# Performance work log

Measured on AMD Instinct MI355X. Metric: run time of the kernel, lower is better.

Reference implementation:

```python
import jax, jax.numpy as jnp
import numpy as np

C = 512
NH = 8
HD = C // NH              # head dim = 64
TOPK = int(HD * 2 / 3)    # keep top-2/3 entries per attention row (DRSformer-style)


def conv2d(x, w, b, groups=1, pad=0):
    y = jax.lax.conv_general_dilated(
        x, w, window_strides=(1, 1), padding=[(pad, pad), (pad, pad)],
        dimension_numbers=('NCHW', 'OIHW', 'NCHW'), feature_group_count=groups)
    return y + b[None, :, None, None]


def setup_inputs() -> dict:
    key = jax.random.key(0)
    ks = jax.random.split(key, 8)
    s = lambda k, sh, fan: jax.random.normal(k, sh, jnp.float32) * (1.0 / np.sqrt(fan))
    return {
        'x': jax.random.normal(ks[0], (2, C, 128, 128), jnp.float32),
        'w_qkv': s(ks[1], (3 * C, C, 1, 1), C),          # 1x1 conv C -> 3C
        'b_qkv': jnp.zeros((3 * C,), jnp.float32),
        'w_dw': s(ks[2], (3 * C, 1, 3, 3), 9),           # 3x3 depthwise on 3C
        'b_dw': jnp.zeros((3 * C,), jnp.float32),
        'scale': jnp.asarray(HD ** -0.5, jnp.float32),   # learned scalar temperature
        'w_proj': s(ks[3], (C, C, 1, 1), C),             # output 1x1 conv
        'b_proj': jnp.zeros((C,), jnp.float32),
    }


def reference(x, w_qkv, b_qkv, w_dw, b_dw, scale, w_proj, b_proj):
    B, _, H, W = x.shape
    # qkv generator: 1x1 conv then 3x3 depthwise conv (Restormer-style)
    qkv = conv2d(x, w_qkv, b_qkv)
    qkv = conv2d(qkv, w_dw, b_dw, groups=3 * C, pad=1)
    q, k, v = jnp.split(qkv, 3, axis=1)
    # b (nh c) h w -> b nh c (h w)
    rs = lambda t: t.reshape(B, NH, HD, H * W)
    q, k, v = rs(q), rs(k), rs(v)
    # L2-normalize along spatial (token) dim
    q = q / jnp.maximum(jnp.linalg.norm(q, axis=-1, keepdims=True), 1e-12)
    k = k / jnp.maximum(jnp.linalg.norm(k, axis=-1, keepdims=True), 1e-12)
    # transposed (channel) attention: [B, NH, HD, HD]
    att = jnp.einsum('bhcn,bhdn->bhcd', q, k) * scale
    # sparsify: keep top-k per row, mask rest to -inf, then softmax
    thresh = jax.lax.top_k(att, TOPK)[0][..., -1:]
    att = jnp.where(att >= thresh, att, -jnp.inf)
    att = jax.nn.softmax(att, axis=-1)
    out = jnp.einsum('bhcd,bhdn->bhcn', att, v)  # [B, NH, HD, HW]
    out = out.reshape(B, C, H, W)
    return conv2d(out, w_proj, b_proj)
```

## Files before the change

kernel.cpp:

```cpp
#include <hip/hip_runtime.h>

typedef unsigned short u16;
typedef _Float16 f16x8 __attribute__((ext_vector_type(8)));
typedef u16 u16x8 __attribute__((ext_vector_type(8)));
typedef u16 u16x4 __attribute__((ext_vector_type(4)));
typedef float f32x4 __attribute__((ext_vector_type(4)));

#define NTOK 16384
#define CCH 512
#define SXN ((long)CCH * NTOK)
#define SQK (512L * NTOK)
#define SQP (1024L * NTOK)
#define SAR 32768L
#define SMB (512L * 512)

__device__ __forceinline__ float h2f(u16 u) {
  _Float16 h = *(_Float16*)&u; return (float)h;
}
__device__ __forceinline__ u16 f2h(float f) {
  _Float16 h = (_Float16)f; return *(u16*)&h;
}
__device__ __forceinline__ void split2(float v, u16& hi, u16& lo) {
  hi = f2h(v); lo = f2h(v - h2f(hi));
}
__device__ __forceinline__ int swz(int row, int ko) { return ko ^ ((row & 7) << 3); }

__device__ __forceinline__ int k2swz(int r, int x) {
  int s = x >> 2, e = x & 3;
  int ps = (((s >> 2) + r) & 7) | ((s & 3) << 3);
  return r * 128 + (ps << 2) + e;
}

__global__ __launch_bounds__(256) void k0_transpose(
    const float* __restrict__ x, u16* __restrict__ xh) {
  __shared__ float ld[64][65];
  const long bz = blockIdx.z;
  x += bz * SXN; xh += bz * SQK;
  const int t = threadIdx.x;
  const int n0 = blockIdx.x * 64, c0 = blockIdx.y * 64;
#pragma unroll
  for (int j = 0; j < 4; ++j) {
    int idx = t + 256 * j;
    int cl = idx >> 4, ns = (idx & 15) * 4;
    float4 v = *(const float4*)(x + (long)(c0 + cl) * NTOK + n0 + ns);
    ld[cl][ns] = v.x; ld[cl][ns + 1] = v.y; ld[cl][ns + 2] = v.z; ld[cl][ns + 3] = v.w;
  }
  __syncthreads();
#pragma unroll
  for (int j = 0; j < 4; ++j) {
    int idx = t + 256 * j;
    int nl = idx >> 4, cs = (idx & 15) * 4;
    u16x4 h;
#pragma unroll
    for (int e = 0; e < 4; ++e) h[e] = f2h(ld[cs + e][nl]);
    *(u16x4*)(xh + (long)(n0 + nl) * CCH + c0 + cs) = h;
  }
}

__global__ __launch_bounds__(256) void k0_cvt_w(const float* __restrict__ a,
                                                u16* __restrict__ oh,
                                                u16* __restrict__ ol) {
  int i = blockIdx.x * 256 + threadIdx.x;
  const float4 v = ((const float4*)a)[i];
  u16 h0, l0, h1, l1, h2, l2, h3, l3;
  split2(v.x, h0, l0); split2(v.y, h1, l1);
  split2(v.z, h2, l2); split2(v.w, h3, l3);
  ((unsigned long long*)oh)[i] = (unsigned long long)h0 | ((unsigned long long)h1 << 16)
                               | ((unsigned long long)h2 << 32) | ((unsigned long long)h3 << 48);
  ((unsigned long long*)ol)[i] = (unsigned long long)l0 | ((unsigned long long)l1 << 16)
                               | ((unsigned long long)l2 << 32) | ((unsigned long long)l3 << 48);
}

__device__ __forceinline__ void storeC(u16* p, float v) { *p = f2h(v); }
__device__ __forceinline__ void storeC(float* p, float v) { *p = v; }

template <typename OutT, bool BIAS_ROW, int GRP, bool GRP_IS_M>
__global__ __launch_bounds__(256) void gemm_bt(
    const u16* __restrict__ A, const u16* __restrict__ B, OutT* __restrict__ C,
    const float* __restrict__ bias, int ldc, long sA, long sB, long sC) {
  const int K = 512;
  __shared__ __align__(16) u16 lA[128 * 64];
  __shared__ __align__(16) u16 lB[128 * 64];
  const long bz = blockIdx.z;
  A += bz * sA; B += bz * sB; C += bz * sC;
  const int t = threadIdx.x;
  const int lane = t & 63, w = t >> 6;
  const int wm = w & 1, wn = w >> 1;
  const int fx = blockIdx.x, fy = blockIdx.y;
  const int gg = fy & (GRP - 1);
  const int go = fx + 8 * (fy / GRP);
  const int bm = (GRP_IS_M ? gg : go) * 128;
  const int bn = (GRP_IS_M ? go : gg) * 128;
  const f32x4 zero4 = {0.f, 0.f, 0.f, 0.f};
  f32x4 acc[4][4];
#pragma unroll
  for (int i = 0; i < 4; ++i)
#pragma unroll
    for (int j = 0; j < 4; ++j) acc[i][j] = zero4;

  for (int kt = 0; kt < K; kt += 64) {
    u16x8 ra[4], rb[4];
#pragma unroll
    for (int j = 0; j < 4; ++j) {
      int idx = t + 256 * j;
      int row = idx >> 3, ko = (idx & 7) << 3;
      ra[j] = *(const u16x8*)(A + (long)(bm + row) * K + kt + ko);
      rb[j] = *(const u16x8*)(B + (long)(bn + row) * K + kt + ko);
    }
    __syncthreads();
#pragma unroll
    for (int j = 0; j < 4; ++j) {
      int idx = t + 256 * j;
      int row = idx >> 3, ko = (idx & 7) << 3;
      *(u16x8*)(&lA[row * 64 + swz(row, ko)]) = ra[j];
      *(u16x8*)(&lB[row * 64 + swz(row, ko)]) = rb[j];
    }
    __syncthreads();
#pragma unroll
    for (int kk = 0; kk < 2; ++kk) {
      f16x8 af[4], bfr[4];
#pragma unroll
      for (int f = 0; f < 4; ++f) {
        int ar = wm * 64 + f * 16 + (lane & 15);
        int br = wn * 64 + f * 16 + (lane & 15);
        int ko = kk * 32 + (lane >> 4) * 8;
        af[f]  = *(const f16x8*)(&lA[ar * 64 + swz(ar, ko)]);
        bfr[f] = *(const f16x8*)(&lB[br * 64 + swz(br, ko)]);
      }
#pragma unroll
      for (int i = 0; i < 4; ++i)
#pragma unroll
        for (int jj = 0; jj < 4; ++jj)
          acc[i][jj] = __builtin_amdgcn_mfma_f32_16x16x32_f16(af[i], bfr[jj], acc[i][jj], 0, 0, 0);
    }
  }
#pragma unroll
  for (int i = 0; i < 4; ++i) {
    const int r0 = bm + wm * 64 + i * 16 + (lane >> 4) * 4;
#pragma unroll
    for (int jj = 0; jj < 4; ++jj) {
      const int c0 = bn + wn * 64 + jj * 16 + (lane & 15);
      const float bcol = BIAS_ROW ? 0.f : bias[c0];
#pragma unroll
      for (int r = 0; r < 4; ++r) {
        float v = acc[i][jj][r] + (BIAS_ROW ? bias[r0 + r] : bcol);
        storeC(&C[(long)(r0 + r) * ldc + c0], v);
      }
    }
  }
}

__global__ __launch_bounds__(256) void gemm_split(
    const u16* __restrict__ Ah, const u16* __restrict__ Al,
    const u16* __restrict__ Bh,
    u16* __restrict__ C, const float* __restrict__ bias, int ldc) {
  const int K = 512;
  __shared__ __align__(16) u16 lAh[128 * 64];
  __shared__ __align__(16) u16 lBh[128 * 64];
  const long bz = blockIdx.z;
  Bh += bz * SQK; C += bz * SQP;
  const int t = threadIdx.x;
  const int lane = t & 63, w = t >> 6;
  const int wm = w & 1, wn = w >> 1;
  const int fx = blockIdx.x, fy = blockIdx.y;
  const int bm = (fy & 7) * 128;
  const int bn = (fx + ((fy >> 3) << 3)) * 128;
  const f32x4 zero4 = {0.f, 0.f, 0.f, 0.f};
  f32x4 acc[4][4];
#pragma unroll
  for (int i = 0; i < 4; ++i)
#pragma unroll
    for (int j = 0; j < 4; ++j) acc[i][j] = zero4;

  const u16* Alp = Al + (long)(bm + wm * 64 + (lane & 15)) * K + ((lane >> 4) << 3);

  for (int kt = 0; kt < K; kt += 64) {
    u16x8 rah[4], rbh[4];
#pragma unroll
    for (int j = 0; j < 4; ++j) {
      int idx = t + 256 * j;
      int row = idx >> 3, ko = (idx & 7) << 3;
      rah[j] = *(const u16x8*)(Ah + (long)(bm + row) * K + kt + ko);
      rbh[j] = *(const u16x8*)(Bh + (long)(bn + row) * K + kt + ko);
    }
    f16x8 afl[2][4];
#pragma unroll
    for (int kk = 0; kk < 2; ++kk)
#pragma unroll
      for (int f = 0; f < 4; ++f)
        afl[kk][f] = *(const f16x8*)(Alp + (long)(f * 16) * K + kt + kk * 32);
    __syncthreads();
#pragma unroll
    for (int j = 0; j < 4; ++j) {
      int idx = t + 256 * j;
      int row = idx >> 3, ko = (idx & 7) << 3;
      *(u16x8*)(&lAh[row * 64 + swz(row, ko)]) = rah[j];
      *(u16x8*)(&lBh[row * 64 + swz(row, ko)]) = rbh[j];
    }
    __syncthreads();
#pragma unroll
    for (int kk = 0; kk < 2; ++kk) {
      f16x8 afh[4], bfh[4];
#pragma unroll
      for (int f = 0; f < 4; ++f) {
        int ar = wm * 64 + f * 16 + (lane & 15);
        int br = wn * 64 + f * 16 + (lane & 15);
        int ko = kk * 32 + (lane >> 4) * 8;
        afh[f] = *(const f16x8*)(&lAh[ar * 64 + swz(ar, ko)]);
        bfh[f] = *(const f16x8*)(&lBh[br * 64 + swz(br, ko)]);
      }
#pragma unroll
      for (int i = 0; i < 4; ++i)
#pragma unroll
        for (int jj = 0; jj < 4; ++jj) {
          acc[i][jj] = __builtin_amdgcn_mfma_f32_16x16x32_f16(afh[i], bfh[jj], acc[i][jj], 0, 0, 0);
          acc[i][jj] = __builtin_amdgcn_mfma_f32_16x16x32_f16(afl[kk][i], bfh[jj], acc[i][jj], 0, 0, 0);
        }
    }
  }
#pragma unroll
  for (int i = 0; i < 4; ++i) {
    const int r0 = bm + wm * 64 + i * 16 + (lane >> 4) * 4;
#pragma unroll
    for (int jj = 0; jj < 4; ++jj) {
      const int c0 = bn + wn * 64 + jj * 16 + (lane & 15);
#pragma unroll
      for (int r = 0; r < 4; ++r) {
        C[(long)(r0 + r) * ldc + c0] = f2h(acc[i][jj][r] + bias[r0 + r]);
      }
    }
  }
}

__global__ __launch_bounds__(256) void k2_qk(
    const u16* __restrict__ qkpre,
    const float* __restrict__ wdw, const float* __restrict__ bdw,
    u16* __restrict__ qh, u16* __restrict__ kh, float* __restrict__ sumsq) {
  __shared__ float st[34 * 128];
  const long bz = blockIdx.z;
  qkpre += bz * SQP; qh += bz * SQK; kh += bz * SQK; sumsq += bz * 1024;
  const int t = threadIdx.x;
  const int s = blockIdx.x;
  const int ch = blockIdx.y;
  const int y0 = s * 32;
  const u16* src = qkpre + (long)ch * NTOK;
  for (int i = t; i < 1088; i += 256) {
    int r = i >> 5, sl = i & 31;
    int gy = y0 - 1 + r;
    float4 v = {0.f, 0.f, 0.f, 0.f};
    if (gy >= 0 && gy < 128) {
      u16x4 h4 = *(const u16x4*)(src + gy * 128 + sl * 4);
      v.x = h2f(h4[0]); v.y = h2f(h4[1]); v.z = h2f(h4[2]); v.w = h2f(h4[3]);
    }
    *(float4*)(&st[k2swz(r, sl * 4)]) = v;
  }
  float wv[9];
#pragma unroll
  for (int i = 0; i < 9; ++i) wv[i] = wdw[ch * 9 + i];
  const float bi = bdw[ch];
  __syncthreads();
  const int y = t >> 3, xg = t & 7, x16 = xg * 16;
  float r0[18], r1[18], r2[18];
#pragma unroll
  for (int k = 0; k < 4; ++k) {
    *(float4*)(&r0[1 + 4 * k]) = *(const float4*)(&st[k2swz(y + 0, x16 + 4 * k)]);
    *(float4*)(&r1[1 + 4 * k]) = *(const float4*)(&st[k2swz(y + 1, x16 + 4 * k)]);
    *(float4*)(&r2[1 + 4 * k]) = *(const float4*)(&st[k2swz(y + 2, x16 + 4 * k)]);
  }
  r0[0]  = (xg > 0) ? st[k2swz(y + 0, x16 - 1)] : 0.f;
  r1[0]  = (xg > 0) ? st[k2swz(y + 1, x16 - 1)] : 0.f;
  r2[0]  = (xg > 0) ? st[k2swz(y + 2, x16 - 1)] : 0.f;
  r0[17] = (xg < 7) ? st[k2swz(y + 0, x16 + 16)] : 0.f;
  r1[17] = (xg < 7) ? st[k2swz(y + 1, x16 + 16)] : 0.f;
  r2[17] = (xg < 7) ? st[k2swz(y + 2, x16 + 16)] : 0.f;
  u16 oh[16];
  float ss = 0.f;
#pragma unroll
  for (int j = 0; j < 16; ++j) {
    float o = bi;
    o += wv[0] * r0[j] + wv[1] * r0[j + 1] + wv[2] * r0[j + 2];
    o += wv[3] * r1[j] + wv[4] * r1[j + 1] + wv[5] * r1[j + 2];
    o += wv[6] * r2[j] + wv[7] * r2[j + 1] + wv[8] * r2[j + 2];
    ss += o * o;
    oh[j] = f2h(o);
  }
  const bool isq = ch < 512;
  u16* dh = isq ? qh : kh;
  const long o = (long)(isq ? ch : ch - 512) * NTOK + (y0 + y) * 128 + x16;
  *(u16x8*)(dh + o)     = *(u16x8*)&oh[0];
  *(u16x8*)(dh + o + 8) = *(u16x8*)&oh[8];
#pragma unroll
  for (int off = 32; off > 0; off >>= 1) ss += __shfl_xor(ss, off);
  if ((t & 63) == 0) atomicAdd(&sumsq[ch], ss);
}

__global__ __launch_bounds__(256) void k2_v(
    const u16* __restrict__ vpre, const float* __restrict__ wdw,
    const float* __restrict__ bdw, u16* __restrict__ vtm) {
  __shared__ __align__(16) u16 st[3 * 66 * 64];
  const long bz = blockIdx.z;
  vpre += bz * SQK; vtm += bz * SQK;
  const int t = threadIdx.x;
  const int xc = blockIdx.x & 1, cc = blockIdx.x >> 1;
  const int y = blockIdx.y;
  const int c0 = cc * 64;
  for (int i = t; i < 1584; i += 256) {
    int l8 = i & 7, dyxi = i >> 3;
    int dy = dyxi / 66, xi = dyxi - dy * 66;
    int yy = y + dy - 1, xx = xc * 64 + xi - 1;
    u16x8 val = {0, 0, 0, 0, 0, 0, 0, 0};
    if (yy >= 0 && yy < 128 && xx >= 0 && xx < 128)
      val = *(const u16x8*)(vpre + (long)(yy * 128 + xx) * 512 + c0 + l8 * 8);
    *(u16x8*)(&st[dyxi * 64 + l8 * 8]) = val;
  }
  __syncthreads();
  const int ch2 = t & 31;
  const int xq = t >> 5;
  const int cga = 1024 + c0 + 2 * ch2;
  float w0[9], w1[9];
#pragma unroll
  for (int i = 0; i < 9; ++i) { w0[i] = wdw[cga * 9 + i]; w1[i] = wdw[(cga + 1) * 9 + i]; }
  const float bi0 = bdw[cga], bi1 = bdw[cga + 1];
  const int nb = y * 128 + xc * 64;
#pragma unroll
  for (int m = 0; m < 8; ++m) {
    int xl = xq * 8 + m;
    float s0 = bi0, s1 = bi1;
#pragma unroll
    for (int dy = 0; dy < 3; ++dy)
#pragma unroll
      for (int dx = 0; dx < 3; ++dx) {
        unsigned int v2 = *(const unsigned int*)(&st[(dy * 66 + xl + dx) * 64 + 2 * ch2]);
        s0 += w0[dy * 3 + dx] * h2f((u16)(v2 & 0xffffu));
        s1 += w1[dy * 3 + dx] * h2f((u16)(v2 >> 16));
      }
    unsigned int pack = (unsigned int)f2h(s0) | ((unsigned int)f2h(s1) << 16);
    *(unsigned int*)(vtm + (long)(nb + xq * 8 + m) * 512 + c0 + 2 * ch2) = pack;
  }
}

__global__ __launch_bounds__(256) void k3_qk(
    const u16* __restrict__ qh, const u16* __restrict__ kh,
    float* __restrict__ att_raw) {
  __shared__ __align__(16) u16 lq[64 * 128];
  __shared__ __align__(16) u16 lk[64 * 128];
  const long bz = blockIdx.z;
  qh += bz * SQK; kh += bz * SQK; att_raw += bz * SAR;
  const int t = threadIdx.x, lane = t & 63, w = t >> 6;
  const int h = blockIdx.y;
  const int n0b = blockIdx.x * 256;
  const u16* qhb = qh + (long)(h * 64) * NTOK;
  const u16* khb = kh + (long)(h * 64) * NTOK;
  const f32x4 zero4 = {0.f, 0.f, 0.f, 0.f};
  f32x4 acc[4] = {zero4, zero4, zero4, zero4};
  for (int ch = 0; ch < 2; ++ch) {
    const int n0 = n0b + ch * 128;
    u16x8 r0[4], r2[4];
#pragma unroll
    for (int j = 0; j < 4; ++j) {
      int idx = t + 256 * j;
      int row = idx >> 4, ko = (idx & 15) << 3;
      long o = (long)row * NTOK + n0 + ko;
      r0[j] = *(const u16x8*)(qhb + o);
      r2[j] = *(const u16x8*)(khb + o);
    }
    __syncthreads();
#pragma unroll
    for (int j = 0; j < 4; ++j) {
      int idx = t + 256 * j;
      int row = idx >> 4, ko = (idx & 15) << 3;
      int sko = swz(row, ko);
      *(u16x8*)(&lq[row * 128 + sko]) = r0[j];
      *(u16x8*)(&lk[row * 128 + sko]) = r2[j];
    }
    __syncthreads();
#pragma unroll
    for (int kk = 0; kk < 4; ++kk) {
      int br = w * 16 + (lane & 15);
      int ko = kk * 32 + (lane >> 4) * 8;
      f16x8 bfh = *(const f16x8*)(&lk[br * 128 + swz(br, ko)]);
#pragma unroll
      for (int f = 0; f < 4; ++f) {
        int ar = f * 16 + (lane & 15);
        f16x8 afh = *(const f16x8*)(&lq[ar * 128 + swz(ar, ko)]);
        acc[f] = __builtin_amdgcn_mfma_f32_16x16x32_f16(afh, bfh, acc[f], 0, 0, 0);
      }
    }
  }
  float* dst = att_raw + h * 64 * 64;
#pragma unroll
  for (int f = 0; f < 4; ++f) {
    int rr = f * 16 + (lane >> 4) * 4;
    int col = w * 16 + (lane & 15);
#pragma unroll
    for (int r = 0; r < 4; ++r) atomicAdd(&dst[(rr + r) * 64 + col], acc[f][r]);
  }
}

__global__ __launch_bounds__(256) void k4_sm(const float* __restrict__ att_raw,
                                             const float* __restrict__ sumsq,
                                             const float* __restrict__ scale_p,
                                             float* __restrict__ att) {
  const long bz = blockIdx.z;
  att_raw += bz * SAR; sumsq += bz * 1024; att += bz * SAR;
  const int t = threadIdx.x, lane = t & 63, w = t >> 6;
  const int row = blockIdx.x * 4 + w;
  const int hi = row >> 6, i = row & 63;
  const float scale = scale_p[0];
  const float nq = fmaxf(sqrtf(sumsq[hi * 64 + i]), 1e-12f);
  const float nk = fmaxf(sqrtf(sumsq[512 + hi * 64 + lane]), 1e-12f);
  float v = att_raw[(long)row * 64 + lane] * scale / (nq * nk);
  int cnt = 0;
  for (int m = 0; m < 64; ++m) {
    float vm = __shfl(v, m);
    cnt += (vm > v || (vm == v && m < lane)) ? 1 : 0;
  }
  unsigned long long ball = __ballot(cnt == 41);
  float thresh = __shfl(v, (int)__builtin_ctzll(ball));
  bool keep = v >= thresh;
  float mx = v;
#pragma unroll
  for (int o = 32; o > 0; o >>= 1) mx = fmaxf(mx, __shfl_xor(mx, o));
  float e = keep ? __expf(v - mx) : 0.f;
  float s = e;
#pragma unroll
  for (int o = 32; o > 0; o >>= 1) s += __shfl_xor(s, o);
  att[(long)row * 64 + lane] = e / s;
}

__global__ __launch_bounds__(256) void k4b_m(const float* __restrict__ att,
                                             const float* __restrict__ wproj,
                                             u16* __restrict__ Mb) {
  __shared__ float wl[64][68];
  __shared__ float al[64][64];
  const long bz = blockIdx.z;
  att += bz * SAR; Mb += bz * SMB;
  const int t = threadIdx.x;
  const int cb = blockIdx.x, h = blockIdx.y;
  const int c0 = cb * 64;
#pragma unroll
  for (int j = 0; j < 4; ++j) {
    int idx = t + 256 * j;
    int r = idx >> 4, c4 = (idx & 15) * 4;
    *(float4*)(&wl[r][c4]) = *(const float4*)(&wproj[(long)(c0 + r) * 512 + h * 64 + c4]);
    *(float4*)(&al[r][c4]) = *(const float4*)(&att[(h * 64 + r) * 64 + c4]);
  }
  __syncthreads();
  const int jd4 = (t & 15) * 4, r0 = t >> 4;
  f32x4 acc[4];
  const f32x4 zero4 = {0.f, 0.f, 0.f, 0.f};
#pragma unroll
  for (int m = 0; m < 4; ++m) acc[m] = zero4;
#pragma unroll
  for (int i2 = 0; i2 < 64; ++i2) {
    f32x4 a4 = *(const f32x4*)(&al[i2][jd4]);
#pragma unroll
    for (int m = 0; m < 4; ++m) {
      float wv = wl[r0 + m * 16][i2];
      acc[m] += wv * a4;
    }
  }
#pragma unroll
  for (int m = 0; m < 4; ++m) {
    u16x4 p;
#pragma unroll
    for (int e = 0; e < 4; ++e) p[e] = f2h(acc[m][e]);
    *(u16x4*)(Mb + (long)(c0 + r0 + m * 16) * 512 + h * 64 + jd4) = p;
  }
}

extern "C" void kernel_launch(void* const* d_in, const int* in_sizes, int n_in,
                              void* d_out, int out_size, void* d_ws, size_t ws_size,
                              hipStream_t stream) {
  (void)in_sizes; (void)n_in; (void)out_size; (void)ws_size;
  const float* x      = (const float*)d_in[0];
  const float* w_qkv  = (const float*)d_in[1];
  const float* b_qkv  = (const float*)d_in[2];
  const float* w_dw   = (const float*)d_in[3];
  const float* b_dw   = (const float*)d_in[4];
  const float* scale  = (const float*)d_in[5];
  const float* w_proj = (const float*)d_in[6];
  const float* b_proj = (const float*)d_in[7];
  float* out = (float*)d_out;
  char* ws = (char*)d_ws;

  u16* qkpre16  = (u16*)(ws + 0L);
  u16* xT_hi    = (u16*)(ws + 67108864L);
  u16* k_hi     = (u16*)(ws + 100663296L);
  u16* vtm      = (u16*)(ws + 134217728L);
  u16* whi      = (u16*)(ws + 167772160L);
  u16* wlo      = (u16*)(ws + 169345024L);
  float* sumsq  = (float*)(ws + 170917888L);
  float* att_raw= (float*)(ws + 170926080L);
  float* att    = (float*)(ws + 171188224L);
  u16* Mb       = (u16*)(ws + 171450368L);
  u16* q_hi = xT_hi;
  u16* vpre = (u16*)d_out;

  k0_cvt_w<<<dim3(768), 256, 0, stream>>>(w_qkv, whi, wlo);
  hipMemsetAsync(sumsq, 0, 8192 + 262144, stream);

  k0_transpose<<<dim3(256, 8, 2), 256, 0, stream>>>(x, xT_hi);
  gemm_split<<<dim3(8, 128, 2), 256, 0, stream>>>(
      whi, wlo, xT_hi, qkpre16, b_qkv, NTOK);
  gemm_bt<u16, false, 4, false><<<dim3(8, 64, 2), 256, 0, stream>>>(
      xT_hi, whi + (long)1024 * 512, vpre, b_qkv + 1024, 512,
      SQK, 0L, SQK);
  k2_qk<<<dim3(4, 1024, 2), 256, 0, stream>>>(
      qkpre16, w_dw, b_dw, q_hi, k_hi, sumsq);
  k2_v<<<dim3(16, 128, 2), 256, 0, stream>>>(vpre, w_dw, b_dw, vtm);
  k3_qk<<<dim3(64, 8, 2), 256, 0, stream>>>(q_hi, k_hi, att_raw);
  k4_sm<<<dim3(128, 1, 2), 256, 0, stream>>>(att_raw, sumsq, scale, att);
  k4b_m<<<dim3(8, 8, 2), 256, 0, stream>>>(att, w_proj, Mb);
  gemm_bt<float, true, 4, true><<<dim3(8, 64, 2), 256, 0, stream>>>(
      Mb, vtm, out, b_proj, NTOK, SMB, SQK, SXN);
}
```

Measured before the change: 262.5 us.

## Load A operand fragments directly from global memory, skipping LDS staging

After: 337.0 us. 28.4% more time.

```diff
diff --git a/kernel.cpp b/kernel.cpp
--- a/kernel.cpp
+++ b/kernel.cpp
@@ -79,7 +79,6 @@
     const u16* __restrict__ A, const u16* __restrict__ B, OutT* __restrict__ C,
     const float* __restrict__ bias, int ldc, long sA, long sB, long sC) {
   const int K = 512;
-  __shared__ __align__(16) u16 lA[128 * 64];
   __shared__ __align__(16) u16 lB[128 * 64];
   const long bz = blockIdx.z;
   A += bz * sA; B += bz * sB; C += bz * sC;
@@ -98,40 +97,44 @@
 #pragma unroll
     for (int j = 0; j < 4; ++j) acc[i][j] = zero4;
 
+  const u16* Ap = A + (long)(bm + wm * 64 + (lane & 15)) * K + ((lane >> 4) << 3);
+
   for (int kt = 0; kt < K; kt += 64) {
-    u16x8 ra[4], rb[4];
+    u16x8 rb[4];
 #pragma unroll
     for (int j = 0; j < 4; ++j) {
       int idx = t + 256 * j;
       int row = idx >> 3, ko = (idx & 7) << 3;
-      ra[j] = *(const u16x8*)(A + (long)(bm + row) * K + kt + ko);
       rb[j] = *(const u16x8*)(B + (long)(bn + row) * K + kt + ko);
     }
+    f16x8 af[2][4];
+#pragma unroll
+    for (int kk = 0; kk < 2; ++kk)
+#pragma unroll
+      for (int f = 0; f < 4; ++f)
+        af[kk][f] = *(const f16x8*)(Ap + (long)(f * 16) * K + kt + kk * 32);
     __syncthreads();
 #pragma unroll
     for (int j = 0; j < 4; ++j) {
       int idx = t + 256 * j;
       int row = idx >> 3, ko = (idx & 7) << 3;
-      *(u16x8*)(&lA[row * 64 + swz(row, ko)]) = ra[j];
       *(u16x8*)(&lB[row * 64 + swz(row, ko)]) = rb[j];
     }
     __syncthreads();
 #pragma unroll
     for (int kk = 0; kk < 2; ++kk) {
-      f16x8 af[4], bfr[4];
+      f16x8 bfr[4];
 #pragma unroll
       for (int f = 0; f < 4; ++f) {
-        int ar = wm * 64 + f * 16 + (lane & 15);
         int br = wn * 64 + f * 16 + (lane & 15);
         int ko = kk * 32 + (lane >> 4) * 8;
-        af[f]  = *(const f16x8*)(&lA[ar * 64 + swz(ar, ko)]);
         bfr[f] = *(const f16x8*)(&lB[br * 64 + swz(br, ko)]);
       }
 #pragma unroll
       for (int i = 0; i < 4; ++i)
 #pragma unroll
         for (int jj = 0; jj < 4; ++jj)
-          acc[i][jj] = __builtin_amdgcn_mfma_f32_16x16x32_f16(af[i], bfr[jj], acc[i][jj], 0, 0, 0);
+          acc[i][jj] = __builtin_amdgcn_mfma_f32_16x16x32_f16(af[kk][i], bfr[jj], acc[i][jj], 0, 0, 0);
     }
   }
 #pragma unroll
@@ -155,7 +158,6 @@
     const u16* __restrict__ Bh,
     u16* __restrict__ C, const float* __restrict__ bias, int ldc) {
   const int K = 512;
-  __shared__ __align__(16) u16 lAh[128 * 64];
   __shared__ __align__(16) u16 lBh[128 * 64];
   const long bz = blockIdx.z;
   Bh += bz * SQK; C += bz * SQP;
@@ -172,48 +174,48 @@
 #pragma unroll
     for (int j = 0; j < 4; ++j) acc[i][j] = zero4;
 
-  const u16* Alp = Al + (long)(bm + wm * 64 + (lane & 15)) * K + ((lane >> 4) << 3);
+  const long arow = (long)(bm + wm * 64 + (lane & 15)) * K + ((lane >> 4) << 3);
+  const u16* Ahp = Ah + arow;
+  const u16* Alp = Al + arow;
 
   for (int kt = 0; kt < K; kt += 64) {
-    u16x8 rah[4], rbh[4];
+    u16x8 rbh[4];
 #pragma unroll
     for (int j = 0; j < 4; ++j) {
       int idx = t + 256 * j;
       int row = idx >> 3, ko = (idx & 7) << 3;
-      rah[j] = *(const u16x8*)(Ah + (long)(bm + row) * K + kt + ko);
       rbh[j] = *(const u16x8*)(Bh + (long)(bn + row) * K + kt + ko);
     }
-    f16x8 afl[2][4];
+    f16x8 afh[2][4], afl[2][4];
 #pragma unroll
     for (int kk = 0; kk < 2; ++kk)
 #pragma unroll
-      for (int f = 0; f < 4; ++f)
+      for (int f = 0; f < 4; ++f) {
+        afh[kk][f] = *(const f16x8*)(Ahp + (long)(f * 16) * K + kt + kk * 32);
         afl[kk][f] = *(const f16x8*)(Alp + (long)(f * 16) * K + kt + kk * 32);
+      }
     __syncthreads();
 #pragma unroll
     for (int j = 0; j < 4; ++j) {
       int idx = t + 256 * j;
       int row = idx >> 3, ko = (idx & 7) << 3;
-      *(u16x8*)(&lAh[row * 64 + swz(row, ko)]) = rah[j];
       *(u16x8*)(&lBh[row * 64 + swz(row, ko)]) = rbh[j];
     }
     __syncthreads();
 #pragma unroll
     for (int kk = 0; kk < 2; ++kk) {
-      f16x8 afh[4], bfh[4];
+      f16x8 bfh[4];
 #pragma unroll
       for (int f = 0; f < 4; ++f) {
-        int ar = wm * 64 + f * 16 + (lane & 15);
         int br = wn * 64 + f * 16 + (lane & 15);
         int ko = kk * 32 + (lane >> 4) * 8;
-        afh[f] = *(const f16x8*)(&lAh[ar * 64 + swz(ar, ko)]);
         bfh[f] = *(const f16x8*)(&lBh[br * 64 + swz(br, ko)]);
       }
 #pragma unroll
       for (int i = 0; i < 4; ++i)
 #pragma unroll
         for (int jj = 0; jj < 4; ++jj) {
-          acc[i][jj] = __builtin_amdgcn_mfma_f32_16x16x32_f16(afh[i], bfh[jj], acc[i][jj], 0, 0, 0);
+          acc[i][jj] = __builtin_amdgcn_mfma_f32_16x16x32_f16(afh[kk][i], bfh[jj], acc[i][jj], 0, 0, 0);
           acc[i][jj] = __builtin_amdgcn_mfma_f32_16x16x32_f16(afl[kk][i], bfh[jj], acc[i][jj], 0, 0, 0);
         }
     }
@@ -342,47 +344,26 @@
 __global__ __launch_bounds__(256) void k3_qk(
     const u16* __restrict__ qh, const u16* __restrict__ kh,
     float* __restrict__ att_raw) {
-  __shared__ __align__(16) u16 lq[64 * 128];
-  __shared__ __align__(16) u16 lk[64 * 128];
   const long bz = blockIdx.z;
   qh += bz * SQK; kh += bz * SQK; att_raw += bz * SAR;
   const int t = threadIdx.x, lane = t & 63, w = t >> 6;
   const int h = blockIdx.y;
   const int n0b = blockIdx.x * 256;
-  const u16* qhb = qh + (long)(h * 64) * NTOK;
-  const u16* khb = kh + (long)(h * 64) * NTOK;
+  const u16* qhb = qh + (long)(h * 64) * NTOK + ((lane >> 4) << 3);
+  const u16* khb = kh + (long)(h * 64 + w * 16 + (lane & 15)) * NTOK + ((lane >> 4) << 3);
+  const u16* qrow = qhb + (long)(lane & 15) * NTOK;
   const f32x4 zero4 = {0.f, 0.f, 0.f, 0.f};
   f32x4 acc[4] = {zero4, zero4, zero4, zero4};
+#pragma unroll
   for (int ch = 0; ch < 2; ++ch) {
     const int n0 = n0b + ch * 128;
-    u16x8 r0[4], r2[4];
-#pragma unroll
-    for (int j = 0; j < 4; ++j) {
-      int idx = t + 256 * j;
-      int row = idx >> 4, ko = (idx & 15) << 3;
-      long o = (long)row * NTOK + n0 + ko;
-      r0[j] = *(const u16x8*)(qhb + o);
-      r2[j] = *(const u16x8*)(khb + o);
-    }
-    __syncthreads();
-#pragma unroll
-    for (int j = 0; j < 4; ++j) {
-      int idx = t + 256 * j;
-      int row = idx >> 4, ko = (idx & 15) << 3;
-      int sko = swz(row, ko);
-      *(u16x8*)(&lq[row * 128 + sko]) = r0[j];
-      *(u16x8*)(&lk[row * 128 + sko]) = r2[j];
-    }
-    __syncthreads();
 #pragma unroll
     for (int kk = 0; kk < 4; ++kk) {
-      int br = w * 16 + (lane & 15);
-      int ko = kk * 32 + (lane >> 4) * 8;
-      f16x8 bfh = *(const f16x8*)(&lk[br * 128 + swz(br, ko)]);
+      const int ko = n0 + kk * 32;
+      f16x8 bfh = *(const f16x8*)(khb + ko);
 #pragma unroll
       for (int f = 0; f < 4; ++f) {
-        int ar = f * 16 + (lane & 15);
-        f16x8 afh = *(const f16x8*)(&lq[ar * 128 + swz(ar, ko)]);
+        f16x8 afh = *(const f16x8*)(qrow + (long)(f * 16) * NTOK + ko);
         acc[f] = __builtin_amdgcn_mfma_f32_16x16x32_f16(afh, bfh, acc[f], 0, 0, 0);
       }
     }
```
